# Performance work log

Hardware: AMD Instinct MI355X
Metric: run time of the kernel (lower is better)

## Reference

```python
import jax, jax.numpy as jnp
import numpy as np
import math

B = 2
D = 256
NH, NL, NP = 8, 4, 4
DH = D // NH
DFF = 1024
NLAYERS = 6
SHAPES = [(96, 96), (48, 48), (24, 24), (12, 12)]
CINS = [256, 512, 768, 1024]
LQ = sum(h * w for h, w in SHAPES)


def setup_inputs() -> dict:
    key = jax.random.key(0)
    ks = iter(jax.random.split(key, 64))
    inp = {}
    for i, (cin, (h, w)) in enumerate(zip(CINS, SHAPES)):
        inp[f"x{i+1}"] = jax.random.normal(next(ks), (B, cin, h, w), jnp.float32)
        inp[f"fc{i+1}_w"] = jax.random.normal(next(ks), (D, cin), jnp.float32) / np.sqrt(cin)
        inp[f"fc{i+1}_b"] = jnp.zeros((D,), jnp.float32)
    inp["gn_g"] = jnp.ones((4, D), jnp.float32)
    inp["gn_b"] = jnp.zeros((4, D), jnp.float32)
    inp["level_embed"] = jax.random.normal(next(ks), (4, D), jnp.float32)
    def lin(k, o, i_, s=1.0):
        return jax.random.normal(k, (NLAYERS, o, i_), jnp.float32) * (s / np.sqrt(i_))
    inp["off_w"] = lin(next(ks), NH * NL * NP * 2, D, 0.01)  # small, like zero-init offsets
    inp["off_b"] = jax.random.normal(next(ks), (NLAYERS, NH * NL * NP * 2), jnp.float32) * 0.5
    inp["aw_w"] = lin(next(ks), NH * NL * NP, D)
    inp["aw_b"] = jnp.zeros((NLAYERS, NH * NL * NP), jnp.float32)
    inp["val_w"] = lin(next(ks), D, D)
    inp["val_b"] = jnp.zeros((NLAYERS, D), jnp.float32)
    inp["out_w"] = lin(next(ks), D, D)
    inp["out_b"] = jnp.zeros((NLAYERS, D), jnp.float32)
    inp["ln1_g"] = jnp.ones((NLAYERS, D), jnp.float32)
    inp["ln1_b"] = jnp.zeros((NLAYERS, D), jnp.float32)
    inp["l1_w"] = lin(next(ks), DFF, D)
    inp["l1_b"] = jnp.zeros((NLAYERS, DFF), jnp.float32)
    inp["l2_w"] = lin(next(ks), D, DFF)
    inp["l2_b"] = jnp.zeros((NLAYERS, D), jnp.float32)
    inp["ln2_g"] = jnp.ones((NLAYERS, D), jnp.float32)
    inp["ln2_b"] = jnp.zeros((NLAYERS, D), jnp.float32)
    return inp


def layer_norm(x, g, b, eps=1e-5):
    m = x.mean(-1, keepdims=True)
    v = ((x - m) ** 2).mean(-1, keepdims=True)
    return (x - m) / jnp.sqrt(v + eps) * g + b


def group_norm(x, g, b, groups=32, eps=1e-5):
    # x: [B, L, C]; torch GroupNorm applied on [B, C, L] -> normalize over (group-channels, L)
    Bq, L, C = x.shape
    xg = x.reshape(Bq, L, groups, C // groups)
    m = xg.mean(axis=(1, 3), keepdims=True)
    v = ((xg - m) ** 2).mean(axis=(1, 3), keepdims=True)
    xg = (xg - m) / jnp.sqrt(v + eps)
    return xg.reshape(Bq, L, C) * g + b


def sine_pos(Hl, Wl):
    # DETR PositionEmbeddingSine, normalize=True, mask all-zero -> cumsum = arange(1..)
    eps, scale, T, npf = 1e-6, 2 * math.pi, 10000.0, D // 2
    ye = (jnp.arange(1, Hl + 1, dtype=jnp.float32) / (Hl + eps)) * scale
    xe = (jnp.arange(1, Wl + 1, dtype=jnp.float32) / (Wl + eps)) * scale
    dim_t = T ** (2 * (jnp.arange(npf) // 2).astype(jnp.float32) / npf)
    def emb(e):
        p = e[:, None] / dim_t
        return jnp.stack([jnp.sin(p[:, 0::2]), jnp.cos(p[:, 1::2])], -1).reshape(-1, npf)
    py, px = emb(ye), emb(xe)
    pos = jnp.concatenate([
        jnp.broadcast_to(py[:, None, :], (Hl, Wl, npf)),
        jnp.broadcast_to(px[None, :, :], (Hl, Wl, npf))], -1)
    return pos.reshape(Hl * Wl, D)


def ref_points():
    # training path: all levels, valid_ratios == 1 (masks all zero)
    refs = []
    for (Hl, Wl) in SHAPES:
        ry = (jnp.arange(Hl, dtype=jnp.float32) + 0.5) / Hl
        rx = (jnp.arange(Wl, dtype=jnp.float32) + 0.5) / Wl
        gy, gx = jnp.meshgrid(ry, rx, indexing='ij')
        refs.append(jnp.stack([gx.ravel(), gy.ravel()], -1))
    r = jnp.concatenate(refs, 0)  # [LQ, 2]
    return jnp.broadcast_to(r[None, :, None, :], (B, LQ, NL, 2))


def ms_deform(value, locs, attw):
    # value: [B, Lin, NH, DH]; locs: [B, Lq, NH, NL, NP, 2] in [0,1]; attw: [B, Lq, NH, NL, NP]
    Bq, Lq = locs.shape[0], locs.shape[1]
    out = jnp.zeros((Bq, Lq, NH, DH), value.dtype)
    start = 0
    for l, (Hl, Wl) in enumerate(SHAPES):
        vf = value[:, start:start + Hl * Wl].transpose(0, 2, 1, 3)  # [B, NH, HW, DH]
        start += Hl * Wl
        loc = locs[:, :, :, l]  # [B, Lq, NH, NP, 2]
        # grid_sample align_corners=False unnormalize: (2u-1+1)/2*W - 0.5 = u*W - 0.5
        x = loc[..., 0] * Wl - 0.5
        y = loc[..., 1] * Hl - 0.5
        x0, y0 = jnp.floor(x), jnp.floor(y)
        tx, ty = x - x0, y - y0
        samp = jnp.zeros((Bq, NH, Lq * NP, DH), value.dtype)
        for dx, dy, w in ((0, 0, (1 - tx) * (1 - ty)), (1, 0, tx * (1 - ty)),
                          (0, 1, (1 - tx) * ty), (1, 1, tx * ty)):
            xi, yi = x0 + dx, y0 + dy
            valid = (xi >= 0) & (xi < Wl) & (yi >= 0) & (yi < Hl)  # zero padding
            idx = (jnp.clip(yi, 0, Hl - 1) * Wl + jnp.clip(xi, 0, Wl - 1)).astype(jnp.int32)
            idxr = idx.transpose(0, 2, 1, 3).reshape(Bq, NH, Lq * NP)
            g = jnp.take_along_axis(vf, idxr[..., None], axis=2)  # [B, NH, Lq*NP, DH]
            wr = (w * valid).transpose(0, 2, 1, 3).reshape(Bq, NH, Lq * NP, 1)
            samp = samp + g * wr
        samp = samp.reshape(Bq, NH, Lq, NP, DH)
        out = out + jnp.einsum('bnqpd,bqnp->bqnd', samp, attw[:, :, :, l])
    return out.reshape(Bq, Lq, NH * DH)


def enc_layer(src, pos, ref, p):
    q = src + pos
    Bq, Lq, _ = src.shape
    off = (q @ p['off_w'].T + p['off_b']).reshape(Bq, Lq, NH, NL, NP, 2)
    aw = jax.nn.softmax((q @ p['aw_w'].T + p['aw_b']).reshape(Bq, Lq, NH, NL * NP), -1)
    aw = aw.reshape(Bq, Lq, NH, NL, NP)
    val = (src @ p['val_w'].T + p['val_b']).reshape(Bq, Lq, NH, DH)
    norml = jnp.array([[w, h] for (h, w) in SHAPES], jnp.float32)  # [NL, 2] as (W, H)
    locs = ref[:, :, None, :, None, :] + off / norml[None, None, None, :, None, :]
    att = ms_deform(val, locs, aw) @ p['out_w'].T + p['out_b']
    src = layer_norm(src + att, p['ln1_g'], p['ln1_b'])
    h = jax.nn.relu(src @ p['l1_w'].T + p['l1_b'])
    src = layer_norm(src + h @ p['l2_w'].T + p['l2_b'], p['ln2_g'], p['ln2_b'])
    return src


LAYER_KEYS = ['off_w', 'off_b', 'aw_w', 'aw_b', 'val_w', 'val_b', 'out_w', 'out_b',
              'ln1_g', 'ln1_b', 'l1_w', 'l1_b', 'l2_w', 'l2_b', 'ln2_g', 'ln2_b']


def _forward(x1, x2, x3, x4, fcs, gn_g, gn_b, level_embed, stacks):
    xs = [x1, x2, x3, x4]
    toks, poss = [], []
    for i, x in enumerate(xs):
        Bq, c, h, w = x.shape
        f = x.reshape(Bq, c, h * w).transpose(0, 2, 1)  # b (h w) c
        t = group_norm(f @ fcs[i][0].T + fcs[i][1], gn_g[i], gn_b[i])
        toks.append(t)
        poss.append(jnp.broadcast_to((sine_pos(h, w) + level_embed[i])[None], (Bq, h * w, D)))
    src = jnp.concatenate(toks, 1)
    pos = jnp.concatenate(poss, 1)
    ref = ref_points()
    for l in range(NLAYERS):
        p = {k: stacks[k][l] for k in LAYER_KEYS}
        src = enc_layer(src, pos, ref, p)
    return src


def reference(x1, x2, x3, x4, fc1_w, fc1_b, fc2_w, fc2_b, fc3_w, fc3_b, fc4_w, fc4_b,
              gn_g, gn_b, level_embed, off_w, off_b, aw_w, aw_b, val_w, val_b, out_w, out_b,
              ln1_g, ln1_b, l1_w, l1_b, l2_w, l2_b, ln2_g, ln2_b):
    fcs = [(fc1_w, fc1_b), (fc2_w, fc2_b), (fc3_w, fc3_b), (fc4_w, fc4_b)]
    stacks = dict(off_w=off_w, off_b=off_b, aw_w=aw_w, aw_b=aw_b, val_w=val_w, val_b=val_b,
                  out_w=out_w, out_b=out_b, ln1_g=ln1_g, ln1_b=ln1_b, l1_w=l1_w, l1_b=l1_b,
                  l2_w=l2_w, l2_b=l2_b, ln2_g=ln2_g, ln2_b=ln2_b)
    src = _forward(x1, x2, x3, x4, fcs, gn_g, gn_b, level_embed, stacks)
    spatial_shapes = jnp.array(SHAPES, jnp.int32)
    level_start_index = jnp.concatenate([jnp.zeros((1,), jnp.int32),
                                         jnp.cumsum(spatial_shapes.prod(1))[:-1]])
    valid_ratios = jnp.ones((B, NL, 2), jnp.float32)
    return (src, level_start_index, spatial_shapes, valid_ratios)
```

## Files before the change

### kernel.cpp

```cpp
#include <hip/hip_runtime.h>
#include <math.h>

#define DD 256
#define DFFN 1024
#define LQT 12240
#define BB 2
#define MROWS (BB * LQT)

typedef __attribute__((ext_vector_type(8))) short short8v;
typedef __attribute__((ext_vector_type(4))) float floatx4;

__device__ __forceinline__ unsigned short f2bf(float x) {
    unsigned int u = __builtin_bit_cast(unsigned int, x);
    u = (u + 0x7fffu + ((u >> 16) & 1u)) >> 16;
    return (unsigned short)u;
}
__device__ __forceinline__ float bf2f(unsigned short h) {
    unsigned int u = ((unsigned int)h) << 16;
    return __builtin_bit_cast(float, u);
}

__device__ __forceinline__ void gload16(const unsigned short* g, unsigned short* lds) {
    __builtin_amdgcn_global_load_lds(
        (const __attribute__((address_space(1))) unsigned int*)g,
        (__attribute__((address_space(3))) unsigned int*)lds, 16, 0, 0);
}

__device__ __forceinline__ void level_of(int q, int& lvl, int& start, int& S) {
    if (q < 9216)       { lvl = 0; start = 0;     S = 96; }
    else if (q < 11520) { lvl = 1; start = 9216;  S = 48; }
    else if (q < 12096) { lvl = 2; start = 11520; S = 24; }
    else                { lvl = 3; start = 12096; S = 12; }
}

__global__ __launch_bounds__(256)
void gemm_qkv(const unsigned short* __restrict__ Aq,
              const unsigned short* __restrict__ Asr,
              const unsigned short* __restrict__ Woff,
              const unsigned short* __restrict__ Waw,
              const unsigned short* __restrict__ Wval,
              const float* __restrict__ boff, const float* __restrict__ baw,
              const float* __restrict__ bval,
              float* __restrict__ awbo, unsigned short* __restrict__ offo,
              unsigned short* __restrict__ valo)
{
    __shared__ alignas(16) unsigned short As[2][4][64][8];
    __shared__ alignas(16) unsigned short Bs[2][4][128][8];
    const int t = threadIdx.x;
    const int m0 = blockIdx.x * 64;
    const int y = blockIdx.y;
    const unsigned short* A; const unsigned short* Wb; const float* bi;
    int nb, mode;
    if (y < 3) {
        A = Aq;
        if (y < 2) { Wb = Woff; bi = boff; nb = y * 128; mode = 0; }
        else       { Wb = Waw;  bi = baw;  nb = 0;       mode = 1; }
    } else {
        A = Asr; Wb = Wval; bi = bval; nb = (y - 3) * 128; mode = 2;
    }
    const int wv = __builtin_amdgcn_readfirstlane(t >> 6);
    const int lane = t & 63;
    const int wm = wv >> 1, wn = wv & 1;
    const int kb = lane >> 4, lr = lane & 15;

    const int ar = min(m0 + lane, MROWS - 1);
    const unsigned short* gA  = A  + (long)ar * 256 + wv * 8;
    const unsigned short* gB0 = Wb + (long)(nb + lane) * 256 + wv * 8;
    const unsigned short* gB1 = Wb + (long)(nb + 64 + lane) * 256 + wv * 8;

    floatx4 acc[2][4];
    #pragma unroll
    for (int m = 0; m < 2; ++m)
        #pragma unroll
        for (int n = 0; n < 4; ++n)
            acc[m][n] = (floatx4){0.f, 0.f, 0.f, 0.f};

    gload16(gA,  &As[0][wv][0][0]);
    gload16(gB0, &Bs[0][wv][0][0]);
    gload16(gB1, &Bs[0][wv][64][0]);
    gA += 32; gB0 += 32; gB1 += 32;
    __syncthreads();

    #pragma unroll
    for (int kt = 0; kt < 8; ++kt) {
        const int cur = kt & 1;
        if (kt < 7) {
            gload16(gA,  &As[cur ^ 1][wv][0][0]);
            gload16(gB0, &Bs[cur ^ 1][wv][0][0]);
            gload16(gB1, &Bs[cur ^ 1][wv][64][0]);
            gA += 32; gB0 += 32; gB1 += 32;
        }
        short8v av[2], bv[4];
        #pragma unroll
        for (int m = 0; m < 2; ++m)
            av[m] = *(const short8v*)&As[cur][kb][wm * 32 + m * 16 + lr][0];
        #pragma unroll
        for (int n = 0; n < 4; ++n)
            bv[n] = *(const short8v*)&Bs[cur][kb][wn * 64 + n * 16 + lr][0];
        #pragma unroll
        for (int m = 0; m < 2; ++m)
            #pragma unroll
            for (int n = 0; n < 4; ++n)
                acc[m][n] = __builtin_amdgcn_mfma_f32_16x16x32_bf16(
                    av[m], bv[n], acc[m][n], 0, 0, 0);
        __syncthreads();
    }

    const int lh = lane >> 4;
    #pragma unroll
    for (int m = 0; m < 2; ++m) {
        const int row0 = m0 + wm * 32 + m * 16 + lh * 4;
        #pragma unroll
        for (int n = 0; n < 4; ++n) {
            const int col = nb + wn * 64 + n * 16 + lr;
            const float b = bi[col];
            #pragma unroll
            for (int r = 0; r < 4; ++r) {
                const int row = row0 + r;
                if (row >= MROWS) continue;
                const float v = acc[m][n][r] + b;
                if (mode == 0)      offo[(long)row * 256 + col] = f2bf(v);
                else if (mode == 1) awbo[(long)row * 128 + col] = v;
                else                valo[(long)row * 256 + col] = f2bf(v);
            }
        }
    }
}

__global__ __launch_bounds__(256)
void gemm64(const unsigned short* __restrict__ A, long aZ,
            const unsigned short* __restrict__ W,
            const float* __restrict__ bias,
            const float* __restrict__ R,
            float* __restrict__ Cf, long cZ, unsigned short* __restrict__ Ch,
            int M, int N, int K, int op)
{
    __shared__ alignas(16) unsigned short As[2][4][64][8];
    __shared__ alignas(16) unsigned short Bs[2][4][128][8];
    const int t = threadIdx.x;
    const int z = blockIdx.z;
    A  += (long)z * aZ;
    if (Cf) Cf += (long)z * cZ;
    const int m0 = blockIdx.x * 64;
    const int n0 = blockIdx.y * 128;
    const int wv = __builtin_amdgcn_readfirstlane(t >> 6);
    const int lane = t & 63;
    const int wm = wv >> 1, wn = wv & 1;
    const int kb = lane >> 4, lr = lane & 15;

    const int ar = min(m0 + lane, M - 1);
    const unsigned short* gA  = A + (long)ar * K + wv * 8;
    const unsigned short* gB0 = W + (long)(n0 + lane) * K + wv * 8;
    const unsigned short* gB1 = W + (long)(n0 + 64 + lane) * K + wv * 8;

    floatx4 acc[2][4];
    #pragma unroll
    for (int m = 0; m < 2; ++m)
        #pragma unroll
        for (int n = 0; n < 4; ++n)
            acc[m][n] = (floatx4){0.f, 0.f, 0.f, 0.f};

    gload16(gA,  &As[0][wv][0][0]);
    gload16(gB0, &Bs[0][wv][0][0]);
    gload16(gB1, &Bs[0][wv][64][0]);
    gA += 32; gB0 += 32; gB1 += 32;
    __syncthreads();

    const int nk = K >> 5;
    for (int kt = 0; kt < nk; ++kt) {
        const int cur = kt & 1;
        if (kt + 1 < nk) {
            gload16(gA,  &As[cur ^ 1][wv][0][0]);
            gload16(gB0, &Bs[cur ^ 1][wv][0][0]);
            gload16(gB1, &Bs[cur ^ 1][wv][64][0]);
            gA += 32; gB0 += 32; gB1 += 32;
        }
        short8v av[2], bv[4];
        #pragma unroll
        for (int m = 0; m < 2; ++m)
            av[m] = *(const short8v*)&As[cur][kb][wm * 32 + m * 16 + lr][0];
        #pragma unroll
        for (int n = 0; n < 4; ++n)
            bv[n] = *(const short8v*)&Bs[cur][kb][wn * 64 + n * 16 + lr][0];
        #pragma unroll
        for (int m = 0; m < 2; ++m)
            #pragma unroll
            for (int n = 0; n < 4; ++n)
                acc[m][n] = __builtin_amdgcn_mfma_f32_16x16x32_bf16(
                    av[m], bv[n], acc[m][n], 0, 0, 0);
        __syncthreads();
    }

    const int lh = lane >> 4;
    #pragma unroll
    for (int m = 0; m < 2; ++m) {
        const int row0 = m0 + wm * 32 + m * 16 + lh * 4;
        #pragma unroll
        for (int n = 0; n < 4; ++n) {
            const int col = n0 + wn * 64 + n * 16 + lr;
            const float b = bias[col];
            #pragma unroll
            for (int r = 0; r < 4; ++r) {
                const int row = row0 + r;
                if (row >= M) continue;
                float v = acc[m][n][r] + b;
                const long o = (long)row * N + col;
                if (op == 0)      Cf[o] = v;
                else if (op == 2) Cf[o] = v + R[o];
                else              Ch[o] = f2bf(v);
            }
        }
    }
}

__global__ __launch_bounds__(256)
void gemm128(const unsigned short* __restrict__ A,
             const unsigned short* __restrict__ W,
             const float* __restrict__ bias, unsigned short* __restrict__ Ch,
             int M, int N, int K)
{
    __shared__ alignas(16) unsigned short As[2][4][128][8];
    __shared__ alignas(16) unsigned short Bs[2][4][128][8];
    const int t = threadIdx.x;
    const int m0 = blockIdx.x * 128;
    const int n0 = blockIdx.y * 128;
    const int wv = __builtin_amdgcn_readfirstlane(t >> 6);
    const int lane = t & 63;
    const int wm = wv >> 1, wn = wv & 1;
    const int kb = lane >> 4, lr = lane & 15;

    const int r0 = min(m0 + lane, M - 1);
    const int r1 = min(m0 + 64 + lane, M - 1);
    const unsigned short* gA0 = A + (long)r0 * K + wv * 8;
    const unsigned short* gA1 = A + (long)r1 * K + wv * 8;
    const unsigned short* gB0 = W + (long)(n0 + lane) * K + wv * 8;
    const unsigned short* gB1 = W + (long)(n0 + 64 + lane) * K + wv * 8;

    floatx4 acc[4][4];
    #pragma unroll
    for (int m = 0; m < 4; ++m)
        #pragma unroll
        for (int n = 0; n < 4; ++n)
            acc[m][n] = (floatx4){0.f, 0.f, 0.f, 0.f};

    gload16(gA0, &As[0][wv][0][0]);
    gload16(gA1, &As[0][wv][64][0]);
    gload16(gB0, &Bs[0][wv][0][0]);
    gload16(gB1, &Bs[0][wv][64][0]);
    gA0 += 32; gA1 += 32; gB0 += 32; gB1 += 32;
    __syncthreads();

    const int nk = K >> 5;
    for (int kt = 0; kt < nk; ++kt) {
        const int cur = kt & 1;
        if (kt + 1 < nk) {
            gload16(gA0, &As[cur ^ 1][wv][0][0]);
            gload16(gA1, &As[cur ^ 1][wv][64][0]);
            gload16(gB0, &Bs[cur ^ 1][wv][0][0]);
            gload16(gB1, &Bs[cur ^ 1][wv][64][0]);
            gA0 += 32; gA1 += 32; gB0 += 32; gB1 += 32;
        }
        short8v av[4], bv[4];
        #pragma unroll
        for (int m = 0; m < 4; ++m)
            av[m] = *(const short8v*)&As[cur][kb][wm * 64 + m * 16 + lr][0];
        #pragma unroll
        for (int n = 0; n < 4; ++n)
            bv[n] = *(const short8v*)&Bs[cur][kb][wn * 64 + n * 16 + lr][0];
        #pragma unroll
        for (int m = 0; m < 4; ++m)
            #pragma unroll
            for (int n = 0; n < 4; ++n)
                acc[m][n] = __builtin_amdgcn_mfma_f32_16x16x32_bf16(
                    av[m], bv[n], acc[m][n], 0, 0, 0);
        __syncthreads();
    }

    const int lh = lane >> 4;
    #pragma unroll
    for (int m = 0; m < 4; ++m) {
        const int row0 = m0 + wm * 64 + m * 16 + lh * 4;
        #pragma unroll
        for (int n = 0; n < 4; ++n) {
            const int col = n0 + wn * 64 + n * 16 + lr;
            const float b = bias[col];
            #pragma unroll
            for (int r = 0; r < 4; ++r) {
                const int row = row0 + r;
                if (row >= M) continue;
                Ch[(long)row * N + col] = f2bf(fmaxf(acc[m][n][r] + b, 0.f));
            }
        }
    }
}

__global__ __launch_bounds__(256)
void tp_k(const float* __restrict__ x, unsigned short* __restrict__ xt,
          int C, int Ml)
{
    __shared__ float tile[32][33];
    const int m0 = blockIdx.x * 32, c0 = blockIdx.y * 32;
    const int zb = blockIdx.z;
    const float* px = x + (long)zb * C * Ml;
    unsigned short* pxt = xt + (long)zb * Ml * C;
    const int t = threadIdx.x;
    {
        const int cl = t >> 3, m4 = (t & 7) * 4;
        const int gm = m0 + m4;
        if (gm < Ml) {
            const float4 v = *(const float4*)(px + (long)(c0 + cl) * Ml + gm);
            tile[cl][m4 + 0] = v.x; tile[cl][m4 + 1] = v.y;
            tile[cl][m4 + 2] = v.z; tile[cl][m4 + 3] = v.w;
        }
    }
    __syncthreads();
    {
        const int ml = t >> 3, c4 = (t & 7) * 4;
        const int gm = m0 + ml;
        if (gm < Ml) {
            ushort4 o;
            o.x = f2bf(tile[c4 + 0][ml]);
            o.y = f2bf(tile[c4 + 1][ml]);
            o.z = f2bf(tile[c4 + 2][ml]);
            o.w = f2bf(tile[c4 + 3][ml]);
            *(ushort4*)(pxt + (long)gm * C + c0 + c4) = o;
        }
    }
}

__global__ __launch_bounds__(256)
void gn_part(const float* __restrict__ src, float* __restrict__ part)
{
    const int x = blockIdx.x;
    const int b = x >> 7, c = x & 127;
    int lvl, chunk;
    if (c < 96)       { lvl = 0; chunk = c; }
    else if (c < 120) { lvl = 1; chunk = c - 96; }
    else if (c < 126) { lvl = 2; chunk = c - 120; }
    else              { lvl = 3; chunk = c - 126; }
    const int starts[4] = {0, 9216, 11520, 12096};
    const int crows[4]  = {96, 96, 96, 72};
    const int rows = crows[lvl];
    const long base = ((long)b * LQT + starts[lvl] + (long)chunk * rows) * DD;
    const int t = threadIdx.x;
    float s = 0.f, sq = 0.f;
    for (int r = 0; r < rows; ++r) {
        const float v = src[base + (long)r * DD + t];
        s += v; sq += v * v;
    }
    #pragma unroll
    for (int o = 1; o < 8; o <<= 1) {
        s  += __shfl_xor(s, o);
        sq += __shfl_xor(sq, o);
    }
    if ((t & 7) == 0) {
        float* p = part + ((long)x * 32 + (t >> 3)) * 2;
        p[0] = s; p[1] = sq;
    }
}

__global__ void gn_fin(const float* __restrict__ part, float* __restrict__ stat)
{
    const int t = threadIdx.x;
    const int b = t >> 7, rest = t & 127;
    const int lvl = rest >> 5, grp = rest & 31;
    const int cbase[4] = {0, 96, 120, 126};
    const int ccnt[4]  = {96, 24, 6, 2};
    const int Ml[4]    = {9216, 2304, 576, 144};
    float s = 0.f, sq = 0.f;
    for (int i = 0; i < ccnt[lvl]; ++i) {
        const float* p = part + ((long)(b * 128 + cbase[lvl] + i) * 32 + grp) * 2;
        s += p[0]; sq += p[1];
    }
    const float cnt = (float)(Ml[lvl] * 8);
    const float mean = s / cnt;
    const float inv = rsqrtf(sq / cnt - mean * mean + 1e-5f);
    float* o = stat + ((b * 4 + lvl) * 32 + grp) * 2;
    o[0] = mean; o[1] = inv;
}

__global__ __launch_bounds__(256)
void gn_apply(float* __restrict__ src, unsigned short* __restrict__ srch,
              unsigned short* __restrict__ qout,
              const float* __restrict__ stat,
              const float* __restrict__ gg, const float* __restrict__ gb,
              const float* __restrict__ pos)
{
    const int t = threadIdx.x;
    const long row = (long)blockIdx.x * 4 + (t >> 6);
    const int lane = t & 63;
    const int b = row >= LQT;
    const int q = (int)row - b * LQT;
    int lvl, start, S;
    level_of(q, lvl, start, S);
    const float2 ms = *(const float2*)(stat + ((b * 4 + lvl) * 32 + (lane >> 1)) * 2);
    const int col = lane * 4;
    const float4 v  = *(const float4*)(src + row * DD + col);
    const float4 gv = *(const float4*)(gg + lvl * DD + col);
    const float4 bv = *(const float4*)(gb + lvl * DD + col);
    float4 y;
    y.x = (v.x - ms.x) * ms.y * gv.x + bv.x;
    y.y = (v.y - ms.x) * ms.y * gv.y + bv.y;
    y.z = (v.z - ms.x) * ms.y * gv.z + bv.z;
    y.w = (v.w - ms.x) * ms.y * gv.w + bv.w;
    *(float4*)(src + row * DD + col) = y;
    ushort4 hh;
    hh.x = f2bf(y.x); hh.y = f2bf(y.y); hh.z = f2bf(y.z); hh.w = f2bf(y.w);
    *(ushort4*)(srch + row * DD + col) = hh;
    const float4 pv = *(const float4*)(pos + (long)q * DD + col);
    ushort4 qq;
    qq.x = f2bf(y.x + pv.x); qq.y = f2bf(y.y + pv.y);
    qq.z = f2bf(y.z + pv.z); qq.w = f2bf(y.w + pv.w);
    *(ushort4*)(qout + row * DD + col) = qq;
}

__global__ __launch_bounds__(256)
void pos_k(float* __restrict__ pos, const float* __restrict__ lemb)
{
    const int q = blockIdx.x;
    const int d = threadIdx.x;
    int lvl, start, S;
    level_of(q, lvl, start, S);
    const int qi = q - start;
    const int r = qi / S, c = qi % S;
    const float twopi = 6.283185307179586f;
    float e; int dd;
    if (d < 128) { e = (float)(r + 1) / ((float)S + 1e-6f) * twopi; dd = d; }
    else         { e = (float)(c + 1) / ((float)S + 1e-6f) * twopi; dd = d - 128; }
    const float dimt = expf(9.210340371976184f * (float)(dd & ~1) / 128.f);
    const float p = e / dimt;
    const float v = (dd & 1) ? cosf(p) : sinf(p);
    pos[(long)q * DD + d] = v + lemb[lvl * DD + d];
}

__global__ __launch_bounds__(256)
void msdeform_k(const unsigned short* __restrict__ val,
                const unsigned short* __restrict__ off,
                const float* __restrict__ aw,
                unsigned short* __restrict__ out)
{
    __shared__ int   s_base[2][128][5];
    __shared__ float s_w[2][128][5];
    const int t = threadIdx.x;
    const int j = t >> 7;
    const int tt = t & 127;
    const int bq = blockIdx.x * 2 + j;
    const int b = bq >= LQT;
    const int q = bq - b * LQT;
    int lvl0, start0, S0;
    level_of(q, lvl0, start0, S0);
    const int qi = q - start0;
    {
        const int lv = (tt >> 2) & 3;
        const int SL[4]  = {96, 48, 24, 12};
        const int STL[4] = {0, 9216, 11520, 12096};
        const int S = SL[lv];
        const float refx = ((float)(qi % S0) + 0.5f) / (float)S0;
        const float refy = ((float)(qi / S0) + 0.5f) / (float)S0;
        const unsigned int ou = *(const unsigned int*)(off + (long)bq * 256 + 2 * tt);
        const float x = refx * (float)S - 0.5f + bf2f((unsigned short)(ou & 0xffffu));
        const float y = refy * (float)S - 0.5f + bf2f((unsigned short)(ou >> 16));
        const float logit = aw[(long)bq * 128 + tt];
        float mx = logit;
        #pragma unroll
        for (int s_ = 1; s_ < 16; s_ <<= 1) mx = fmaxf(mx, __shfl_xor(mx, s_));
        const float e = __expf(logit - mx);
        float sum = e;
        #pragma unroll
        for (int s_ = 1; s_ < 16; s_ <<= 1) sum += __shfl_xor(sum, s_);
        const float wat = e / sum;
        const float x0 = floorf(x), y0 = floorf(y);
        const float tx = x - x0, ty = y - y0;
        const int ix = (int)x0, iy = (int)y0;
        #pragma unroll
        for (int c = 0; c < 4; ++c) {
            const int dx = c & 1, dy = c >> 1;
            const int xi = ix + dx, yi = iy + dy;
            const bool ok = (xi >= 0) && (xi < S) && (yi >= 0) && (yi < S);
            const int cx = min(max(xi, 0), S - 1);
            const int cy = min(max(yi, 0), S - 1);
            const float wxy = (dx ? tx : 1.f - tx) * (dy ? ty : 1.f - ty);
            s_base[j][tt][c] = (STL[lv] + cy * S + cx) * 256;
            s_w[j][tt][c] = ok ? wxy * wat : 0.f;
        }
    }
    __syncthreads();
    const int h = tt >> 4, d8 = (tt >> 2) & 3, sub = tt & 3;
    const unsigned short* vb = val + (long)b * (LQT * DD) + h * 32 + d8 * 8;
    float a0 = 0.f, a1 = 0.f, a2 = 0.f, a3 = 0.f;
    float a4 = 0.f, a5 = 0.f, a6 = 0.f, a7 = 0.f;
    #pragma unroll
    for (int i = 0; i < 4; ++i) {
        const int task = h * 16 + i * 4 + sub;
        #pragma unroll
        for (int c = 0; c < 4; ++c) {
            const float wv = s_w[j][task][c];
            const uint4 g = *(const uint4*)(vb + s_base[j][task][c]);
            a0 = fmaf(wv, bf2f((unsigned short)(g.x & 0xffffu)), a0);
            a1 = fmaf(wv, bf2f((unsigned short)(g.x >> 16)), a1);
            a2 = fmaf(wv, bf2f((unsigned short)(g.y & 0xffffu)), a2);
            a3 = fmaf(wv, bf2f((unsigned short)(g.y >> 16)), a3);
            a4 = fmaf(wv, bf2f((unsigned short)(g.z & 0xffffu)), a4);
            a5 = fmaf(wv, bf2f((unsigned short)(g.z >> 16)), a5);
            a6 = fmaf(wv, bf2f((unsigned short)(g.w & 0xffffu)), a6);
            a7 = fmaf(wv, bf2f((unsigned short)(g.w >> 16)), a7);
        }
    }
    #pragma unroll
    for (int o = 1; o < 4; o <<= 1) {
        a0 += __shfl_xor(a0, o); a1 += __shfl_xor(a1, o);
        a2 += __shfl_xor(a2, o); a3 += __shfl_xor(a3, o);
        a4 += __shfl_xor(a4, o); a5 += __shfl_xor(a5, o);
        a6 += __shfl_xor(a6, o); a7 += __shfl_xor(a7, o);
    }
    if (sub == 0) {
        uint4 o;
        o.x = (unsigned)f2bf(a0) | ((unsigned)f2bf(a1) << 16);
        o.y = (unsigned)f2bf(a2) | ((unsigned)f2bf(a3) << 16);
        o.z = (unsigned)f2bf(a4) | ((unsigned)f2bf(a5) << 16);
        o.w = (unsigned)f2bf(a6) | ((unsigned)f2bf(a7) << 16);
        *(uint4*)(out + (long)bq * DD + h * 32 + d8 * 8) = o;
    }
}

__global__ __launch_bounds__(256)
void layernorm_k(const float* __restrict__ x, const float* __restrict__ g,
                 const float* __restrict__ b, float* __restrict__ outf,
                 unsigned short* __restrict__ outh,
                 const float* __restrict__ pos, unsigned short* __restrict__ qout)
{
    const int t = threadIdx.x;
    const long row = (long)blockIdx.x * 4 + (t >> 6);
    const int lane = t & 63;
    const float4 v = *(const float4*)(x + row * DD + lane * 4);
    float s  = v.x + v.y + v.z + v.w;
    float sq = v.x * v.x + v.y * v.y + v.z * v.z + v.w * v.w;
    #pragma unroll
    for (int o = 1; o < 64; o <<= 1) {
        s  += __shfl_xor(s, o);
        sq += __shfl_xor(sq, o);
    }
    const float mean = s * (1.f / 256.f);
    const float inv = rsqrtf(sq * (1.f / 256.f) - mean * mean + 1e-5f);
    const float4 gv = *(const float4*)(g + lane * 4);
    const float4 bv = *(const float4*)(b + lane * 4);
    float4 y;
    y.x = (v.x - mean) * inv * gv.x + bv.x;
    y.y = (v.y - mean) * inv * gv.y + bv.y;
    y.z = (v.z - mean) * inv * gv.z + bv.z;
    y.w = (v.w - mean) * inv * gv.w + bv.w;
    *(float4*)(outf + row * DD + lane * 4) = y;
    ushort4 hh;
    hh.x = f2bf(y.x); hh.y = f2bf(y.y); hh.z = f2bf(y.z); hh.w = f2bf(y.w);
    *(ushort4*)(outh + row * DD + lane * 4) = hh;
    if (qout) {
        const int qrow = (int)row - (row >= LQT ? LQT : 0);
        const float4 pv = *(const float4*)(pos + (long)qrow * DD + lane * 4);
        ushort4 qq;
        qq.x = f2bf(y.x + pv.x); qq.y = f2bf(y.y + pv.y);
        qq.z = f2bf(y.z + pv.z); qq.w = f2bf(y.w + pv.w);
        *(ushort4*)(qout + row * DD + lane * 4) = qq;
    }
}

#define WCVT_TOTAL 5177344L
__global__ __launch_bounds__(256)
void wcvt_k(const float* __restrict__ s0, const float* __restrict__ s1,
            const float* __restrict__ s2, const float* __restrict__ s3,
            const float* __restrict__ s4, const float* __restrict__ s5,
            const float* __restrict__ s6, const float* __restrict__ s7,
            const float* __restrict__ s8, const float* __restrict__ s9,
            unsigned short* __restrict__ dst)
{
    const long i = ((long)blockIdx.x * 256 + threadIdx.x) * 4;
    if (i >= WCVT_TOTAL) return;
    const float* sp; long base;
    if (i < 1048576) {
        if (i < 655360) {
            if (i < 65536)       { sp = s0; base = 0; }
            else if (i < 196608) { sp = s1; base = 65536; }
            else if (i < 393216) { sp = s2; base = 196608; }
            else                 { sp = s3; base = 393216; }
        } else                   { sp = s4; base = 655360; }
    } else if (i < 2031616) {
        if (i < 1245184)         { sp = s5; base = 1048576; }
        else if (i < 1638400)    { sp = s6; base = 1245184; }
        else                     { sp = s7; base = 1638400; }
    } else if (i < 3604480)      { sp = s8; base = 2031616; }
    else                         { sp = s9; base = 3604480; }
    const float4 v = *(const float4*)(sp + (i - base));
    ushort4 o;
    o.x = f2bf(v.x); o.y = f2bf(v.y); o.z = f2bf(v.z); o.w = f2bf(v.w);
    *(ushort4*)(dst + i) = o;
}

__global__ void tail_k(float* __restrict__ o)
{
    const float tv[28] = {0.f, 9216.f, 11520.f, 12096.f,
                          96.f, 96.f, 48.f, 48.f, 24.f, 24.f, 12.f, 12.f,
                          1.f, 1.f, 1.f, 1.f, 1.f, 1.f, 1.f, 1.f,
                          1.f, 1.f, 1.f, 1.f, 1.f, 1.f, 1.f, 1.f};
    const int t = threadIdx.x;
    if (t < 28) o[t] = tv[t];
}

extern "C" void kernel_launch(void* const* d_in, const int* in_sizes, int n_in,
                              void* d_out, int out_size, void* d_ws, size_t ws_size,
                              hipStream_t stream)
{
    const float* xs[4]  = {(const float*)d_in[0], (const float*)d_in[3],
                           (const float*)d_in[6], (const float*)d_in[9]};
    const float* fcw[4] = {(const float*)d_in[1], (const float*)d_in[4],
                           (const float*)d_in[7], (const float*)d_in[10]};
    const float* fcb[4] = {(const float*)d_in[2], (const float*)d_in[5],
                           (const float*)d_in[8], (const float*)d_in[11]};
    const float* gn_g = (const float*)d_in[12];
    const float* gn_b = (const float*)d_in[13];
    const float* lemb = (const float*)d_in[14];
    const float* off_w = (const float*)d_in[15];
    const float* off_b = (const float*)d_in[16];
    const float* aw_w  = (const float*)d_in[17];
    const float* aw_b  = (const float*)d_in[18];
    const float* val_w = (const float*)d_in[19];
    const float* val_b = (const float*)d_in[20];
    const float* out_w = (const float*)d_in[21];
    const float* out_b = (const float*)d_in[22];
    const float* ln1_g = (const float*)d_in[23];
    const float* ln1_b = (const float*)d_in[24];
    const float* l1_w  = (const float*)d_in[25];
    const float* l1_b  = (const float*)d_in[26];
    const float* l2_w  = (const float*)d_in[27];
    const float* l2_b  = (const float*)d_in[28];
    const float* ln2_g = (const float*)d_in[29];
    const float* ln2_b = (const float*)d_in[30];

    float* src = (float*)d_out;
    float* ws = (float*)d_ws;
    float* pos = ws;
    float* awb = pos + 3133440;
    float* tmp = awb + 3133440;
    unsigned short* xt = (unsigned short*)tmp;
    unsigned short* q_bf   = (unsigned short*)(tmp + 6266880);
    unsigned short* off_bf = q_bf   + 6266880;
    unsigned short* val_bf = off_bf + 6266880;
    unsigned short* msd_bf = val_bf + 6266880;
    unsigned short* hid_bf = q_bf;
    unsigned short* src_bf = msd_bf + 6266880;
    unsigned short* wb     = src_bf + 6266880;
    unsigned short* wb_fc[4];
    wb_fc[0] = wb;
    wb_fc[1] = wb_fc[0] + 65536;
    wb_fc[2] = wb_fc[1] + 131072;
    wb_fc[3] = wb_fc[2] + 196608;
    unsigned short* wb_off = wb_fc[3] + 262144;
    unsigned short* wb_aw  = wb_off + 393216;
    unsigned short* wb_val = wb_aw  + 196608;
    unsigned short* wb_out = wb_val + 393216;
    unsigned short* wb_l1  = wb_out + 393216;
    unsigned short* wb_l2  = wb_l1  + 1572864;
    float* part = (float*)(wb_l2 + 1572864);
    float* stat = part + 16384;
    (void)in_sizes; (void)n_in; (void)out_size; (void)ws_size;

    const int CINS[4]   = {256, 512, 768, 1024};
    const int SS[4]     = {96, 48, 24, 12};
    const int STARTS[4] = {0, 9216, 11520, 12096};
    const long XTOFF[4] = {0, 4718592, 7077888, 7962624};

    pos_k<<<LQT, 256, 0, stream>>>(pos, lemb);
    wcvt_k<<<(WCVT_TOTAL / 4 + 255) / 256, 256, 0, stream>>>(
        fcw[0], fcw[1], fcw[2], fcw[3], off_w, aw_w, val_w, out_w, l1_w, l2_w, wb);

    for (int i = 0; i < 4; ++i) {
        const int Ml = SS[i] * SS[i];
        tp_k<<<dim3((Ml + 31) / 32, CINS[i] / 32, BB), 256, 0, stream>>>(
            xs[i], xt + XTOFF[i], CINS[i], Ml);
    }
    for (int i = 0; i < 4; ++i) {
        const int Ml = SS[i] * SS[i];
        gemm64<<<dim3((Ml + 63) / 64, 2, BB), 256, 0, stream>>>(
            xt + XTOFF[i], (long)Ml * CINS[i],
            wb_fc[i], fcb[i], nullptr,
            src + (long)STARTS[i] * DD, (long)LQT * DD, nullptr,
            Ml, DD, CINS[i], 0);
    }
    gn_part<<<256, 256, 0, stream>>>(src, part);
    gn_fin<<<1, 256, 0, stream>>>(part, stat);
    gn_apply<<<MROWS / 4, 256, 0, stream>>>(src, src_bf, q_bf, stat, gn_g, gn_b, pos);

    for (int l = 0; l < 6; ++l) {
        gemm_qkv<<<dim3(383, 5), 256, 0, stream>>>(
            q_bf, src_bf,
            wb_off + (long)l * 65536, wb_aw + (long)l * 32768,
            wb_val + (long)l * 65536,
            off_b + l * DD, aw_b + l * 128, val_b + l * DD,
            awb, off_bf, val_bf);
        msdeform_k<<<MROWS / 2, 256, 0, stream>>>(val_bf, off_bf, awb, msd_bf);
        gemm64<<<dim3(383, 2), 256, 0, stream>>>(
            msd_bf, 0, wb_out + (long)l * 65536, out_b + l * DD, src,
            tmp, 0, nullptr, MROWS, DD, DD, 2);
        layernorm_k<<<MROWS / 4, 256, 0, stream>>>(
            tmp, ln1_g + l * DD, ln1_b + l * DD, src, src_bf, nullptr, nullptr);
        gemm128<<<dim3(192, 8), 256, 0, stream>>>(
            src_bf, wb_l1 + (long)l * 262144, l1_b + l * DFFN, hid_bf,
            MROWS, DFFN, DD);
        gemm64<<<dim3(383, 2), 256, 0, stream>>>(
            hid_bf, 0, wb_l2 + (long)l * 262144, l2_b + l * DD, src,
            tmp, 0, nullptr, MROWS, DD, DFFN, 2);
        const bool last = (l == 5);
        layernorm_k<<<MROWS / 4, 256, 0, stream>>>(
            tmp, ln2_g + l * DD, ln2_b + l * DD, src, src_bf,
            last ? nullptr : pos, last ? nullptr : q_bf);
    }
    tail_k<<<1, 32, 0, stream>>>(src + (long)BB * LQT * DD);
}
```

Before: 1.629 ms.

## Fuse residual add and LayerNorm into full-width output and FFN GEMMs

Adds a gemm_ln kernel in which each block computes a 64x256 tile covering a full row, adds bias and residual, and computes the LayerNorm statistics in-block. The output and FFN2 projections then write normalized fp32/bf16 (and pos-added query) results directly, removing the fp32 tmp round trip and the separate layernorm launches. The msdeform block index is also permuted to spread queries across blocks, and workspace buffers are re-aliased. In exchange there is lower grid parallelism (383 blocks), more registers per thread, and the residual R is read in place while the same rows of src are overwritten. This is safe only because each block touches its own rows.

```diff
diff --git a/kernel.cpp b/kernel.cpp
--- a/kernel.cpp
+++ b/kernel.cpp
@@ -131,16 +131,15 @@
 void gemm64(const unsigned short* __restrict__ A, long aZ,
             const unsigned short* __restrict__ W,
             const float* __restrict__ bias,
-            const float* __restrict__ R,
-            float* __restrict__ Cf, long cZ, unsigned short* __restrict__ Ch,
-            int M, int N, int K, int op)
+            float* __restrict__ Cf, long cZ,
+            int M, int N, int K)
 {
     __shared__ alignas(16) unsigned short As[2][4][64][8];
     __shared__ alignas(16) unsigned short Bs[2][4][128][8];
     const int t = threadIdx.x;
     const int z = blockIdx.z;
     A  += (long)z * aZ;
-    if (Cf) Cf += (long)z * cZ;
+    Cf += (long)z * cZ;
     const int m0 = blockIdx.x * 64;
     const int n0 = blockIdx.y * 128;
     const int wv = __builtin_amdgcn_readfirstlane(t >> 6);
@@ -203,11 +202,7 @@
             for (int r = 0; r < 4; ++r) {
                 const int row = row0 + r;
                 if (row >= M) continue;
-                float v = acc[m][n][r] + b;
-                const long o = (long)row * N + col;
-                if (op == 0)      Cf[o] = v;
-                else if (op == 2) Cf[o] = v + R[o];
-                else              Ch[o] = f2bf(v);
+                Cf[(long)row * N + col] = acc[m][n][r] + b;
             }
         }
     }
@@ -289,6 +284,140 @@
                 const int row = row0 + r;
                 if (row >= M) continue;
                 Ch[(long)row * N + col] = f2bf(fmaxf(acc[m][n][r] + b, 0.f));
+            }
+        }
+    }
+}
+
+__global__ __launch_bounds__(256)
+void gemm_ln(const unsigned short* __restrict__ A,
+             const unsigned short* __restrict__ W,
+             const float* __restrict__ bias, const float* R,
+             const float* __restrict__ lg, const float* __restrict__ lb,
+             float* outf, unsigned short* __restrict__ outh,
+             const float* __restrict__ pos, unsigned short* __restrict__ qout,
+             int M, int K)
+{
+    __shared__ alignas(16) unsigned short As[2][4][64][8];
+    __shared__ alignas(16) unsigned short Bs[2][4][256][8];
+    __shared__ float red[64][4][2];
+    __shared__ float smean[64], sinv[64];
+    const int t = threadIdx.x;
+    const int m0 = blockIdx.x * 64;
+    const int wv = __builtin_amdgcn_readfirstlane(t >> 6);
+    const int lane = t & 63;
+    const int kb = lane >> 4, lr = lane & 15;
+    const int lh = kb;
+
+    const int ar = min(m0 + lane, M - 1);
+    const unsigned short* gA  = A + (long)ar * K + wv * 8;
+    const unsigned short* gB0 = W + (long)lane * K + wv * 8;
+    const unsigned short* gB1 = W + (long)(64 + lane) * K + wv * 8;
+    const unsigned short* gB2 = W + (long)(128 + lane) * K + wv * 8;
+    const unsigned short* gB3 = W + (long)(192 + lane) * K + wv * 8;
+
+    floatx4 acc[4][4];
+    #pragma unroll
+    for (int m = 0; m < 4; ++m)
+        #pragma unroll
+        for (int n = 0; n < 4; ++n)
+            acc[m][n] = (floatx4){0.f, 0.f, 0.f, 0.f};
+
+    gload16(gA,  &As[0][wv][0][0]);
+    gload16(gB0, &Bs[0][wv][0][0]);
+    gload16(gB1, &Bs[0][wv][64][0]);
+    gload16(gB2, &Bs[0][wv][128][0]);
+    gload16(gB3, &Bs[0][wv][192][0]);
+    gA += 32; gB0 += 32; gB1 += 32; gB2 += 32; gB3 += 32;
+    __syncthreads();
+
+    const int nk = K >> 5;
+    for (int kt = 0; kt < nk; ++kt) {
+        const int cur = kt & 1;
+        if (kt + 1 < nk) {
+            gload16(gA,  &As[cur ^ 1][wv][0][0]);
+            gload16(gB0, &Bs[cur ^ 1][wv][0][0]);
+            gload16(gB1, &Bs[cur ^ 1][wv][64][0]);
+            gload16(gB2, &Bs[cur ^ 1][wv][128][0]);
+            gload16(gB3, &Bs[cur ^ 1][wv][192][0]);
+            gA += 32; gB0 += 32; gB1 += 32; gB2 += 32; gB3 += 32;
+        }
+        short8v av[4], bv[4];
+        #pragma unroll
+        for (int m = 0; m < 4; ++m)
+            av[m] = *(const short8v*)&As[cur][kb][m * 16 + lr][0];
+        #pragma unroll
+        for (int n = 0; n < 4; ++n)
+            bv[n] = *(const short8v*)&Bs[cur][kb][wv * 64 + n * 16 + lr][0];
+        #pragma unroll
+        for (int m = 0; m < 4; ++m)
+            #pragma unroll
+            for (int n = 0; n < 4; ++n)
+                acc[m][n] = __builtin_amdgcn_mfma_f32_16x16x32_bf16(
+                    av[m], bv[n], acc[m][n], 0, 0, 0);
+        __syncthreads();
+    }
+
+    #pragma unroll
+    for (int n = 0; n < 4; ++n) {
+        const int col = wv * 64 + n * 16 + lr;
+        const float bcol = bias[col];
+        #pragma unroll
+        for (int m = 0; m < 4; ++m) {
+            #pragma unroll
+            for (int r = 0; r < 4; ++r) {
+                const int grow = m0 + m * 16 + lh * 4 + r;
+                const int rr = min(grow, M - 1);
+                acc[m][n][r] += bcol + R[(long)rr * 256 + col];
+            }
+        }
+    }
+    #pragma unroll
+    for (int m = 0; m < 4; ++m) {
+        #pragma unroll
+        for (int r = 0; r < 4; ++r) {
+            float s = acc[m][0][r] + acc[m][1][r] + acc[m][2][r] + acc[m][3][r];
+            float q = acc[m][0][r] * acc[m][0][r] + acc[m][1][r] * acc[m][1][r]
+                    + acc[m][2][r] * acc[m][2][r] + acc[m][3][r] * acc[m][3][r];
+            #pragma unroll
+            for (int o = 1; o < 16; o <<= 1) {
+                s += __shfl_xor(s, o);
+                q += __shfl_xor(q, o);
+            }
+            if (lr == 0) {
+                red[m * 16 + lh * 4 + r][wv][0] = s;
+                red[m * 16 + lh * 4 + r][wv][1] = q;
+            }
+        }
+    }
+    __syncthreads();
+    if (t < 64) {
+        const float s = red[t][0][0] + red[t][1][0] + red[t][2][0] + red[t][3][0];
+        const float q = red[t][0][1] + red[t][1][1] + red[t][2][1] + red[t][3][1];
+        const float mean = s * (1.f / 256.f);
+        smean[t] = mean;
+        sinv[t] = rsqrtf(q * (1.f / 256.f) - mean * mean + 1e-5f);
+    }
+    __syncthreads();
+    #pragma unroll
+    for (int n = 0; n < 4; ++n) {
+        const int col = wv * 64 + n * 16 + lr;
+        const float gc = lg[col], bc = lb[col];
+        #pragma unroll
+        for (int m = 0; m < 4; ++m) {
+            #pragma unroll
+            for (int r = 0; r < 4; ++r) {
+                const int row = m * 16 + lh * 4 + r;
+                const int grow = m0 + row;
+                if (grow >= M) continue;
+                const float y = (acc[m][n][r] - smean[row]) * sinv[row] * gc + bc;
+                const long o = (long)grow * 256 + col;
+                outf[o] = y;
+                outh[o] = f2bf(y);
+                if (qout) {
+                    const int qrow = grow - (grow >= LQT ? LQT : 0);
+                    qout[o] = f2bf(y + pos[(long)qrow * 256 + col]);
+                }
             }
         }
     }
@@ -444,7 +573,9 @@
     const int t = threadIdx.x;
     const int j = t >> 7;
     const int tt = t & 127;
-    const int bq = blockIdx.x * 2 + j;
+    const int bid = blockIdx.x;
+    const int sb = (bid & 7) * 1530 + (bid >> 3);
+    const int bq = sb * 2 + j;
     const int b = bq >= LQT;
     const int q = bq - b * LQT;
     int lvl0, start0, S0;
@@ -520,46 +651,6 @@
         o.z = (unsigned)f2bf(a4) | ((unsigned)f2bf(a5) << 16);
         o.w = (unsigned)f2bf(a6) | ((unsigned)f2bf(a7) << 16);
         *(uint4*)(out + (long)bq * DD + h * 32 + d8 * 8) = o;
-    }
-}
-
-__global__ __launch_bounds__(256)
-void layernorm_k(const float* __restrict__ x, const float* __restrict__ g,
-                 const float* __restrict__ b, float* __restrict__ outf,
-                 unsigned short* __restrict__ outh,
-                 const float* __restrict__ pos, unsigned short* __restrict__ qout)
-{
-    const int t = threadIdx.x;
-    const long row = (long)blockIdx.x * 4 + (t >> 6);
-    const int lane = t & 63;
-    const float4 v = *(const float4*)(x + row * DD + lane * 4);
-    float s  = v.x + v.y + v.z + v.w;
-    float sq = v.x * v.x + v.y * v.y + v.z * v.z + v.w * v.w;
-    #pragma unroll
-    for (int o = 1; o < 64; o <<= 1) {
-        s  += __shfl_xor(s, o);
-        sq += __shfl_xor(sq, o);
-    }
-    const float mean = s * (1.f / 256.f);
-    const float inv = rsqrtf(sq * (1.f / 256.f) - mean * mean + 1e-5f);
-    const float4 gv = *(const float4*)(g + lane * 4);
-    const float4 bv = *(const float4*)(b + lane * 4);
-    float4 y;
-    y.x = (v.x - mean) * inv * gv.x + bv.x;
-    y.y = (v.y - mean) * inv * gv.y + bv.y;
-    y.z = (v.z - mean) * inv * gv.z + bv.z;
-    y.w = (v.w - mean) * inv * gv.w + bv.w;
-    *(float4*)(outf + row * DD + lane * 4) = y;
-    ushort4 hh;
-    hh.x = f2bf(y.x); hh.y = f2bf(y.y); hh.z = f2bf(y.z); hh.w = f2bf(y.w);
-    *(ushort4*)(outh + row * DD + lane * 4) = hh;
-    if (qout) {
-        const int qrow = (int)row - (row >= LQT ? LQT : 0);
-        const float4 pv = *(const float4*)(pos + (long)qrow * DD + lane * 4);
-        ushort4 qq;
-        qq.x = f2bf(y.x + pv.x); qq.y = f2bf(y.y + pv.y);
-        qq.z = f2bf(y.z + pv.z); qq.w = f2bf(y.w + pv.w);
-        *(ushort4*)(qout + row * DD + lane * 4) = qq;
     }
 }
 
@@ -638,14 +729,14 @@
     float* ws = (float*)d_ws;
     float* pos = ws;
     float* awb = pos + 3133440;
-    float* tmp = awb + 3133440;
-    unsigned short* xt = (unsigned short*)tmp;
-    unsigned short* q_bf   = (unsigned short*)(tmp + 6266880);
-    unsigned short* off_bf = q_bf   + 6266880;
-    unsigned short* val_bf = off_bf + 6266880;
-    unsigned short* msd_bf = val_bf + 6266880;
-    unsigned short* hid_bf = q_bf;
-    unsigned short* src_bf = msd_bf + 6266880;
+    unsigned short* bigbuf = (unsigned short*)(awb + 3133440);
+    unsigned short* xt     = bigbuf;
+    unsigned short* off_bf = bigbuf;
+    unsigned short* val_bf = bigbuf + 6266880;
+    unsigned short* msd_bf = bigbuf + 12533760;
+    unsigned short* hid_bf = bigbuf;
+    unsigned short* q_bf   = bigbuf + 25067520;
+    unsigned short* src_bf = q_bf + 6266880;
     unsigned short* wb     = src_bf + 6266880;
     unsigned short* wb_fc[4];
     wb_fc[0] = wb;
@@ -680,9 +771,9 @@
         const int Ml = SS[i] * SS[i];
         gemm64<<<dim3((Ml + 63) / 64, 2, BB), 256, 0, stream>>>(
             xt + XTOFF[i], (long)Ml * CINS[i],
-            wb_fc[i], fcb[i], nullptr,
-            src + (long)STARTS[i] * DD, (long)LQT * DD, nullptr,
-            Ml, DD, CINS[i], 0);
+            wb_fc[i], fcb[i],
+            src + (long)STARTS[i] * DD, (long)LQT * DD,
+            Ml, DD, CINS[i]);
     }
     gn_part<<<256, 256, 0, stream>>>(src, part);
     gn_fin<<<1, 256, 0, stream>>>(part, stat);
@@ -696,21 +787,18 @@
             off_b + l * DD, aw_b + l * 128, val_b + l * DD,
             awb, off_bf, val_bf);
         msdeform_k<<<MROWS / 2, 256, 0, stream>>>(val_bf, off_bf, awb, msd_bf);
-        gemm64<<<dim3(383, 2), 256, 0, stream>>>(
-            msd_bf, 0, wb_out + (long)l * 65536, out_b + l * DD, src,
-            tmp, 0, nullptr, MROWS, DD, DD, 2);
-        layernorm_k<<<MROWS / 4, 256, 0, stream>>>(
-            tmp, ln1_g + l * DD, ln1_b + l * DD, src, src_bf, nullptr, nullptr);
+        gemm_ln<<<383, 256, 0, stream>>>(
+            msd_bf, wb_out + (long)l * 65536, out_b + l * DD, src,
+            ln1_g + l * DD, ln1_b + l * DD, src, src_bf,
+            nullptr, nullptr, MROWS, DD);
         gemm128<<<dim3(192, 8), 256, 0, stream>>>(
             src_bf, wb_l1 + (long)l * 262144, l1_b + l * DFFN, hid_bf,
             MROWS, DFFN, DD);
-        gemm64<<<dim3(383, 2), 256, 0, stream>>>(
-            hid_bf, 0, wb_l2 + (long)l * 262144, l2_b + l * DD, src,
-            tmp, 0, nullptr, MROWS, DD, DFFN, 2);
         const bool last = (l == 5);
-        layernorm_k<<<MROWS / 4, 256, 0, stream>>>(
-            tmp, ln2_g + l * DD, ln2_b + l * DD, src, src_bf,
-            last ? nullptr : pos, last ? nullptr : q_bf);
+        gemm_ln<<<383, 256, 0, stream>>>(
+            hid_bf, wb_l2 + (long)l * 262144, l2_b + l * DD, src,
+            ln2_g + l * DD, ln2_b + l * DD, src, src_bf,
+            last ? nullptr : pos, last ? nullptr : q_bf, MROWS, DFFN);
     }
     tail_k<<<1, 32, 0, stream>>>(src + (long)BB * LQT * DD);
 }
```

New measurement: 1.637 ms. About the same (+0.5%).
